# Kernel tuning notes

Measured on AMD Instinct MI355X. Metric: run time of the kernel, lower is better.

The kernel has to match this reference:

```python
import jax, jax.numpy as jnp
import numpy as np

N_HEADS = 8
D_HEAD = 64
SCALE = D_HEAD ** -0.5


def setup_inputs() -> dict:
    key = jax.random.key(0)
    k1, k2, k3 = jax.random.split(key, 3)
    B, H, W, C = 16, 32, 32, 512
    ft = jax.random.normal(k1, (B, H, W, C), dtype=jnp.float32)
    # Dense layers: to_qkv -> n_heads*n_dim_heads*3 = 1536 units, to_out -> n_channels
    w_qkv = jax.random.normal(k2, (C, N_HEADS * D_HEAD * 3), dtype=jnp.float32) * (C ** -0.5)
    b_qkv = jnp.zeros((N_HEADS * D_HEAD * 3,), dtype=jnp.float32)
    w_out = jax.random.normal(k3, (N_HEADS * D_HEAD, C), dtype=jnp.float32) * ((N_HEADS * D_HEAD) ** -0.5)
    b_out = jnp.zeros((C,), dtype=jnp.float32)
    return {"ft": ft, "w_qkv": w_qkv, "b_qkv": b_qkv, "w_out": w_out, "b_out": b_out}


def reference(ft, w_qkv, b_qkv, w_out, b_out):
    B, H, W, C = ft.shape
    N = H * W
    x = ft.reshape(B, N, C)                       # b (h w) c
    qkv = x @ w_qkv + b_qkv                       # b n (heads * 3*d_head)
    qkv = qkv.reshape(B, N, N_HEADS, 3 * D_HEAD)  # 'b x (h d) -> b x h d'
    q, k, v = jnp.split(qkv, 3, axis=-1)          # each: b n heads d_head
    attn = jnp.einsum('bxhd,byhd->bxyh', q, k) * SCALE
    attn = jax.nn.softmax(attn, axis=2)           # softmax over key axis y
    res = jnp.einsum('bxyh,byhd->bxhd', attn, v)  # b x h d
    res = res.reshape(B, N, N_HEADS * D_HEAD)     # 'b x h d -> b x (h d)'
    res = res @ w_out + b_out
    res = res + x                                 # residual with pre-qkv flattened input
    return res.reshape(B, H, W, C)
```

## Files before the change

### kernel.cpp

```cpp
#include <hip/hip_runtime.h>
#include <hip/hip_bf16.h>

using u16 = unsigned short;
using u32 = unsigned int;
typedef __attribute__((ext_vector_type(8))) short short8;
typedef __attribute__((ext_vector_type(4))) float f32x4;

#define MFMA16(A, B, C) __builtin_amdgcn_mfma_f32_16x16x32_bf16((A), (B), (C), 0, 0, 0)

__device__ __forceinline__ u16 f2bf(float f) {
  union { float f; u32 i; } v; v.f = f;
  u32 x = v.i;
  return (u16)((x + 0x7fffu + ((x >> 16) & 1u)) >> 16);
}
__device__ __forceinline__ u32 pkbf(float a, float b) {
  union { __hip_bfloat162 h; u32 u; } v;
  v.h = __float22bfloat162_rn(make_float2(a, b));
  return v.u;
}
__device__ __forceinline__ void gl16(const u16* g, u16* l) {
  __builtin_amdgcn_global_load_lds(
      (const __attribute__((address_space(1))) u32*)g,
      (__attribute__((address_space(3))) u32*)l, 16, 0, 0);
}

__global__ __launch_bounds__(256) void conv_x(const float* __restrict__ X,
                                              u16* __restrict__ Xbf) {
  const int i = (blockIdx.x * 256 + threadIdx.x) * 8;
  float4 a = *(const float4*)(X + i);
  float4 b = *(const float4*)(X + i + 4);
  uint4 o;
  o.x = pkbf(a.x, a.y); o.y = pkbf(a.z, a.w);
  o.z = pkbf(b.x, b.y); o.w = pkbf(b.z, b.w);
  *(uint4*)(Xbf + i) = o;
}

__global__ __launch_bounds__(256) void transpose_w(
    const float* __restrict__ Wq, const float* __restrict__ Wo,
    u16* __restrict__ Wqt, u16* __restrict__ Wot) {
  const int z = blockIdx.z;
  if (z == 1 && blockIdx.x >= 16) return;
  const float* src = z ? Wo : Wq;
  u16* dst = z ? Wot : Wqt;
  const int ncols = z ? 512 : 1536;
  __shared__ float tile[32][33];
  const int t = threadIdx.x;
  const int kt = blockIdx.y * 32, nt = blockIdx.x * 32;
  const int r = t >> 3, c4 = (t & 7) * 4;
  float4 v = *(const float4*)(src + (size_t)(kt + r) * ncols + nt + c4);
  tile[r][c4 + 0] = v.x; tile[r][c4 + 1] = v.y;
  tile[r][c4 + 2] = v.z; tile[r][c4 + 3] = v.w;
  __syncthreads();
  uint2 p = make_uint2(pkbf(tile[c4 + 0][r], tile[c4 + 1][r]),
                       pkbf(tile[c4 + 2][r], tile[c4 + 3][r]));
  *(uint2*)(dst + (size_t)(nt + r) * 512 + kt + c4) = p;
}

__global__ __launch_bounds__(256) void qkv_gemm(
    const u16* __restrict__ Xbf, const u16* __restrict__ Wt,
    const float* __restrict__ Bias,
    u16* __restrict__ Qp, u16* __restrict__ Kp, u16* __restrict__ Vt) {
  __shared__ u16 Xs[128][32];
  __shared__ u16 Ws[128][32];
  const int t = threadIdx.x;
  const int bm = blockIdx.y * 128, bn = blockIdx.x * 128;
  const int w = t >> 6, lane = t & 63, quad = lane >> 4, l16 = lane & 15;
  const int mtb = (w >> 1) * 64, ntb = (w & 1) * 64;
  const int rr = lane >> 2;
  const int gch = ((lane & 3) ^ ((lane >> 3) & 3)) * 8;
  const int sw = (quad ^ ((l16 >> 1) & 3)) * 8;

  const u16* xg0 = Xbf + (size_t)(bm + w * 16 + rr) * 512 + gch;
  const u16* xg1 = xg0 + (size_t)64 * 512;
  const u16* wg0 = Wt + (size_t)(bn + w * 16 + rr) * 512 + gch;
  const u16* wg1 = wg0 + (size_t)64 * 512;
  u16* xl0 = &Xs[w * 16][0]; u16* xl1 = &Xs[64 + w * 16][0];
  u16* wl0 = &Ws[w * 16][0]; u16* wl1 = &Ws[64 + w * 16][0];

  f32x4 acc[4][4];
  const f32x4 z4 = {0.f, 0.f, 0.f, 0.f};
  #pragma unroll
  for (int mi = 0; mi < 4; mi++)
    #pragma unroll
    for (int ni = 0; ni < 4; ni++) acc[mi][ni] = z4;

  for (int k0 = 0; k0 < 512; k0 += 32) {
    gl16(xg0 + k0, xl0);
    gl16(xg1 + k0, xl1);
    gl16(wg0 + k0, wl0);
    gl16(wg1 + k0, wl1);
    __syncthreads();
    short8 af[4], bf4[4];
    #pragma unroll
    for (int mi = 0; mi < 4; mi++)
      af[mi] = *(const short8*)&Xs[mtb + mi * 16 + l16][sw];
    #pragma unroll
    for (int ni = 0; ni < 4; ni++)
      bf4[ni] = *(const short8*)&Ws[ntb + ni * 16 + l16][sw];
    #pragma unroll
    for (int mi = 0; mi < 4; mi++)
      #pragma unroll
      for (int ni = 0; ni < 4; ni++)
        acc[mi][ni] = MFMA16(af[mi], bf4[ni], acc[mi][ni]);
    __syncthreads();
  }

  #pragma unroll
  for (int ni = 0; ni < 4; ni++) {
    const int g = bn + ntb + ni * 16;
    const int h = g / 192, rm = g % 192;
    const int type = rm >> 6, dbase = rm & 63;
    const float bias = Bias[g + l16];
    const float qsc = (type == 0) ? 0.125f * 1.44269504088896340736f : 1.0f;
    #pragma unroll
    for (int mi = 0; mi < 4; mi++) {
      const int row0 = bm + mtb + mi * 16 + quad * 4;
      const int b = row0 >> 10, n0 = row0 & 1023;
      const size_t bh = (size_t)(b * 8 + h) * 65536;
      if (type == 2) {
        uint2 p = make_uint2(pkbf(acc[mi][ni][0] + bias, acc[mi][ni][1] + bias),
                             pkbf(acc[mi][ni][2] + bias, acc[mi][ni][3] + bias));
        *(uint2*)(Vt + bh + (size_t)(dbase + l16) * 1024 + n0) = p;
      } else {
        u16* dst = (type ? Kp : Qp) + bh;
        #pragma unroll
        for (int r = 0; r < 4; r++)
          dst[(size_t)(n0 + r) * 64 + dbase + l16] =
              f2bf((acc[mi][ni][r] + bias) * qsc);
      }
    }
  }
}

__global__ __launch_bounds__(512, 6) void attn_mfma(
    const u16* __restrict__ Qp, const u16* __restrict__ Kp,
    const u16* __restrict__ Vt, u16* __restrict__ ATT) {
  __shared__ u16 Ks[128][64];
  __shared__ u16 Vs[64][128];
  const int t = threadIdx.x, w = t >> 6, lane = t & 63;
  const int quad = lane >> 4, l16 = lane & 15;
  const int bx = blockIdx.x;
  const int c = bx & 7, g = bx >> 3;
  const int qt = g & 7, u = g >> 3;
  const int bh_id = u * 8 + c;
  const int b = bh_id >> 3, h = bh_id & 7;
  const size_t bh = (size_t)bh_id * 65536;
  const u16* Qb = Qp + bh;
  const u16* Kb = Kp + bh;
  const u16* Vb = Vt + bh;
  const int q0 = qt * 128 + w * 16;

  const u16* kgA = Kb + (size_t)(t >> 3) * 64 + ((t & 7) ^ ((t >> 3) & 7)) * 8;
  const u16* kgB = kgA + (size_t)64 * 64;
  const u16* vgA = Vb + (size_t)(t >> 4) * 1024 + ((t & 15) ^ ((t >> 4) & 7)) * 8;
  const u16* vgB = vgA + (size_t)32 * 1024;
  u16* ksl0 = &Ks[0][0] + w * 512;  u16* ksl1 = ksl0 + 4096;
  u16* vsl0 = &Vs[0][0] + w * 512;  u16* vsl1 = vsl0 + 4096;

  const int m7 = l16 & 7;
  const char* ksb = (const char*)&Ks[0][0];
  const char* vsb = (const char*)&Vs[0][0];
  const int kb0 = l16 * 128 + (quad ^ m7) * 16;
  const int kb1 = kb0 ^ 64;
  int vo[4];
  #pragma unroll
  for (int ks = 0; ks < 4; ks++)
    vo[ks] = l16 * 256 + ((4 * ks + quad) ^ m7) * 16;

  short8 qf[2];
  #pragma unroll
  for (int ks = 0; ks < 2; ks++)
    qf[ks] = *(const short8*)(Qb + (size_t)(q0 + l16) * 64 + ks * 32 + quad * 8);

  float l_ = 0.f;
  f32x4 Of[4];
  const f32x4 z4 = {0.f, 0.f, 0.f, 0.f};
  #pragma unroll
  for (int ni = 0; ni < 4; ni++) Of[ni] = z4;

  for (int kt = 0; kt < 8; kt++) {
    __syncthreads();
    gl16(kgA + kt * 8192, ksl0);
    gl16(kgB + kt * 8192, ksl1);
    gl16(vgA + kt * 128,  vsl0);
    gl16(vgB + kt * 128,  vsl1);
    __syncthreads();

    u32 e[8], o[8];
    #pragma unroll
    for (int nt = 0; nt < 8; nt++) {
      short8 k0f = *(const short8*)(ksb + kb0 + nt * 2048);
      short8 k1f = *(const short8*)(ksb + kb1 + nt * 2048);
      f32x4 s = z4;
      s = MFMA16(k0f, qf[0], s);
      s = MFMA16(k1f, qf[1], s);
      float p0 = __builtin_amdgcn_exp2f(s[0]);
      float p1 = __builtin_amdgcn_exp2f(s[1]);
      float p2 = __builtin_amdgcn_exp2f(s[2]);
      float p3 = __builtin_amdgcn_exp2f(s[3]);
      l_ += (p0 + p1) + (p2 + p3);
      const u32 lo = pkbf(p0, p1), hi = pkbf(p2, p3);
      if (nt & 1) { o[(nt >> 1) * 2] = lo; o[(nt >> 1) * 2 + 1] = hi; }
      else        { e[(nt >> 1) * 2] = lo; e[(nt >> 1) * 2 + 1] = hi; }
    }
    #pragma unroll
    for (int i = 0; i < 8; i++) {
      auto t01 = __builtin_amdgcn_permlane32_swap(e[i], o[i], false, false);
      auto xy  = __builtin_amdgcn_permlane16_swap(t01[0], t01[1], false, false);
      e[i] = xy[0]; o[i] = xy[1];
    }
    #pragma unroll
    for (int ks = 0; ks < 4; ks++) {
      union { short8 v; u32 u[4]; } pa;
      pa.u[0] = e[2 * ks]; pa.u[1] = e[2 * ks + 1];
      pa.u[2] = o[2 * ks]; pa.u[3] = o[2 * ks + 1];
      #pragma unroll
      for (int ni = 0; ni < 4; ni++) {
        short8 vf = *(const short8*)(vsb + vo[ks] + ni * 4096);
        Of[ni] = MFMA16(pa.v, vf, Of[ni]);
      }
    }
  }
  l_ += __shfl_xor(l_, 16);
  l_ += __shfl_xor(l_, 32);
  float lv[4];
  #pragma unroll
  for (int r = 0; r < 4; r++) lv[r] = __shfl(l_, quad * 4 + r);
  #pragma unroll
  for (int r = 0; r < 4; r++) {
    const float inv = 1.0f / lv[r];
    const int row = b * 1024 + q0 + quad * 4 + r;
    #pragma unroll
    for (int ni = 0; ni < 4; ni++)
      ATT[(size_t)row * 512 + h * 64 + ni * 16 + l16] = f2bf(Of[ni][r] * inv);
  }
}

__global__ __launch_bounds__(256) void out_proj(
    const u16* __restrict__ A, const u16* __restrict__ Wt,
    const float* __restrict__ Bias, const float* __restrict__ FT,
    float* __restrict__ OUT) {
  __shared__ u16 As[128][32];
  __shared__ u16 Ws[128][32];
  const int t = threadIdx.x;
  const int bm = blockIdx.y * 128, bn = blockIdx.x * 128;
  const int w = t >> 6, lane = t & 63, quad = lane >> 4, l16 = lane & 15;
  const int mtb = (w >> 1) * 64, ntb = (w & 1) * 64;
  const int rr = lane >> 2;
  const int gch = ((lane & 3) ^ ((lane >> 3) & 3)) * 8;
  const int sw = (quad ^ ((l16 >> 1) & 3)) * 8;

  const u16* ag0 = A + (size_t)(bm + w * 16 + rr) * 512 + gch;
  const u16* ag1 = ag0 + (size_t)64 * 512;
  const u16* wg0 = Wt + (size_t)(bn + w * 16 + rr) * 512 + gch;
  const u16* wg1 = wg0 + (size_t)64 * 512;
  u16* al0 = &As[w * 16][0]; u16* al1 = &As[64 + w * 16][0];
  u16* wl0 = &Ws[w * 16][0]; u16* wl1 = &Ws[64 + w * 16][0];

  f32x4 acc[4][4];
  const f32x4 z4 = {0.f, 0.f, 0.f, 0.f};
  #pragma unroll
  for (int mi = 0; mi < 4; mi++)
    #pragma unroll
    for (int ni = 0; ni < 4; ni++) acc[mi][ni] = z4;

  for (int k0 = 0; k0 < 512; k0 += 32) {
    gl16(ag0 + k0, al0);
    gl16(ag1 + k0, al1);
    gl16(wg0 + k0, wl0);
    gl16(wg1 + k0, wl1);
    __syncthreads();
    short8 af[4], bf4[4];
    #pragma unroll
    for (int mi = 0; mi < 4; mi++)
      af[mi] = *(const short8*)&As[mtb + mi * 16 + l16][sw];
    #pragma unroll
    for (int ni = 0; ni < 4; ni++)
      bf4[ni] = *(const short8*)&Ws[ntb + ni * 16 + l16][sw];
    #pragma unroll
    for (int mi = 0; mi < 4; mi++)
      #pragma unroll
      for (int ni = 0; ni < 4; ni++)
        acc[mi][ni] = MFMA16(af[mi], bf4[ni], acc[mi][ni]);
    __syncthreads();
  }

  #pragma unroll
  for (int ni = 0; ni < 4; ni++) {
    const int g = bn + ntb + ni * 16;
    const float bias = Bias[g + l16];
    #pragma unroll
    for (int mi = 0; mi < 4; mi++) {
      const int row0 = bm + mtb + mi * 16 + quad * 4;
      #pragma unroll
      for (int r = 0; r < 4; r++) {
        const size_t idx = (size_t)(row0 + r) * 512 + g + l16;
        OUT[idx] = acc[mi][ni][r] + bias + FT[idx];
      }
    }
  }
}

extern "C" void kernel_launch(void* const* d_in, const int* in_sizes, int n_in,
                              void* d_out, int out_size, void* d_ws, size_t ws_size,
                              hipStream_t stream) {
  const float* ft    = (const float*)d_in[0];
  const float* w_qkv = (const float*)d_in[1];
  const float* b_qkv = (const float*)d_in[2];
  const float* w_out = (const float*)d_in[3];
  const float* b_out = (const float*)d_in[4];
  float* out = (float*)d_out;

  char* p = (char*)d_ws;
  u16* Xbf    = (u16*)(p);
  u16* ATT    = Xbf;
  u16* Wqkv_t = (u16*)(p + 16777216);
  u16* Wout_t = (u16*)(p + 18350080);
  u16* Qp     = (u16*)(p + 18874368);
  u16* Kp     = (u16*)(p + 35651584);
  u16* Vt     = (u16*)(p + 52428800);

  conv_x     <<<4096, 256, 0, stream>>>(ft, Xbf);
  transpose_w<<<dim3(48, 16, 2), 256, 0, stream>>>(w_qkv, w_out, Wqkv_t, Wout_t);
  qkv_gemm   <<<dim3(12, 128), 256, 0, stream>>>(Xbf, Wqkv_t, b_qkv, Qp, Kp, Vt);
  attn_mfma  <<<dim3(1024), 512, 0, stream>>>(Qp, Kp, Vt, ATT);
  out_proj   <<<dim3(4, 128), 256, 0, stream>>>(ATT, Wout_t, b_out, ft, out);
}
```

Baseline: 205.5 us.

## Double-buffer K/V tiles in LDS and raise wave priority around MFMA

The attention kernel now keeps two LDS buffers for K and V. It prefetches the next key tile with async global-to-LDS loads while the current tile is being computed, which cuts one barrier per iteration and hides load latency. It also raises the wave priority with s_setprio around the MFMA sections and fully unrolls the key loop. The cost is double the LDS per block and a lower launch-bounds occupancy hint, so fewer blocks can be resident per CU to hide latency.

```diff
diff --git a/kernel.cpp b/kernel.cpp
--- a/kernel.cpp
+++ b/kernel.cpp
@@ -132,11 +132,11 @@
   }
 }
 
-__global__ __launch_bounds__(512, 6) void attn_mfma(
+__global__ __launch_bounds__(512, 4) void attn_mfma(
     const u16* __restrict__ Qp, const u16* __restrict__ Kp,
     const u16* __restrict__ Vt, u16* __restrict__ ATT) {
-  __shared__ u16 Ks[128][64];
-  __shared__ u16 Vs[64][128];
+  __shared__ u16 Ks[2][128][64];
+  __shared__ u16 Vs[2][64][128];
   const int t = threadIdx.x, w = t >> 6, lane = t & 63;
   const int quad = lane >> 4, l16 = lane & 15;
   const int bx = blockIdx.x;
@@ -154,12 +154,14 @@
   const u16* kgB = kgA + (size_t)64 * 64;
   const u16* vgA = Vb + (size_t)(t >> 4) * 1024 + ((t & 15) ^ ((t >> 4) & 7)) * 8;
   const u16* vgB = vgA + (size_t)32 * 1024;
-  u16* ksl0 = &Ks[0][0] + w * 512;  u16* ksl1 = ksl0 + 4096;
-  u16* vsl0 = &Vs[0][0] + w * 512;  u16* vsl1 = vsl0 + 4096;
+  u16* ks0 = &Ks[0][0][0] + w * 512;
+  u16* ks1 = &Ks[1][0][0] + w * 512;
+  u16* vs0 = &Vs[0][0][0] + w * 512;
+  u16* vs1 = &Vs[1][0][0] + w * 512;
 
   const int m7 = l16 & 7;
-  const char* ksb = (const char*)&Ks[0][0];
-  const char* vsb = (const char*)&Vs[0][0];
+  const char* ksb = (const char*)&Ks[0][0][0];
+  const char* vsb = (const char*)&Vs[0][0][0];
   const int kb0 = l16 * 128 + (quad ^ m7) * 16;
   const int kb1 = kb0 ^ 64;
   int vo[4];
@@ -178,19 +180,29 @@
   #pragma unroll
   for (int ni = 0; ni < 4; ni++) Of[ni] = z4;
 
+  gl16(kgA, ks0); gl16(kgB, ks0 + 4096);
+  gl16(vgA, vs0); gl16(vgB, vs0 + 4096);
+  __syncthreads();
+
+  #pragma unroll
   for (int kt = 0; kt < 8; kt++) {
-    __syncthreads();
-    gl16(kgA + kt * 8192, ksl0);
-    gl16(kgB + kt * 8192, ksl1);
-    gl16(vgA + kt * 128,  vsl0);
-    gl16(vgB + kt * 128,  vsl1);
-    __syncthreads();
+    const int cur = kt & 1;
+    if (kt < 7) {
+      u16* kd = cur ? ks0 : ks1;
+      u16* vd = cur ? vs0 : vs1;
+      gl16(kgA + (kt + 1) * 8192, kd);
+      gl16(kgB + (kt + 1) * 8192, kd + 4096);
+      gl16(vgA + (kt + 1) * 128,  vd);
+      gl16(vgB + (kt + 1) * 128,  vd + 4096);
+    }
+    const int co = cur * 16384;
 
     u32 e[8], o[8];
+    __builtin_amdgcn_s_setprio(1);
     #pragma unroll
     for (int nt = 0; nt < 8; nt++) {
-      short8 k0f = *(const short8*)(ksb + kb0 + nt * 2048);
-      short8 k1f = *(const short8*)(ksb + kb1 + nt * 2048);
+      short8 k0f = *(const short8*)(ksb + co + kb0 + nt * 2048);
+      short8 k1f = *(const short8*)(ksb + co + kb1 + nt * 2048);
       f32x4 s = z4;
       s = MFMA16(k0f, qf[0], s);
       s = MFMA16(k1f, qf[1], s);
@@ -203,12 +215,14 @@
       if (nt & 1) { o[(nt >> 1) * 2] = lo; o[(nt >> 1) * 2 + 1] = hi; }
       else        { e[(nt >> 1) * 2] = lo; e[(nt >> 1) * 2 + 1] = hi; }
     }
+    __builtin_amdgcn_s_setprio(0);
     #pragma unroll
     for (int i = 0; i < 8; i++) {
       auto t01 = __builtin_amdgcn_permlane32_swap(e[i], o[i], false, false);
       auto xy  = __builtin_amdgcn_permlane16_swap(t01[0], t01[1], false, false);
       e[i] = xy[0]; o[i] = xy[1];
     }
+    __builtin_amdgcn_s_setprio(1);
     #pragma unroll
     for (int ks = 0; ks < 4; ks++) {
       union { short8 v; u32 u[4]; } pa;
@@ -216,10 +230,12 @@
       pa.u[2] = o[2 * ks]; pa.u[3] = o[2 * ks + 1];
       #pragma unroll
       for (int ni = 0; ni < 4; ni++) {
-        short8 vf = *(const short8*)(vsb + vo[ks] + ni * 4096);
+        short8 vf = *(const short8*)(vsb + co + vo[ks] + ni * 4096);
         Of[ni] = MFMA16(pa.v, vf, Of[ni]);
       }
     }
+    __builtin_amdgcn_s_setprio(0);
+    __syncthreads();
   }
   l_ += __shfl_xor(l_, 16);
   l_ += __shfl_xor(l_, 32);
```

Result: slower. 332.5 us (+61.8%).
